# Kernel optimization log

Measured on AMD Instinct MI355X. Metric: run time of the kernel, lower is better.

The kernel has to match this reference:

```python
import jax, jax.numpy as jnp
import numpy as np

N = 50000      # nodes
E = 800000     # edges
IN_DIM = 256
H = 128
OUT_DIM = 64
DEPTH = 3
NEG_SLOPE = 0.2  # DGL GATConv default leaky_relu slope


def setup_inputs() -> dict:
    key = jax.random.key(0)
    ks = jax.random.split(key, 20)
    def nrm(k, shape, fan_in):
        return jax.random.normal(k, shape, jnp.float32) / jnp.sqrt(jnp.float32(fan_in))
    x = jax.random.normal(ks[0], (N, IN_DIM), jnp.float32)
    src = jax.random.randint(ks[1], (E,), 0, N, jnp.int32)
    dst = jax.random.randint(ks[2], (E,), 0, N, jnp.int32)
    # weights stored as [in, out] (y = x @ W + b)
    inp = dict(
        x=x, src=src, dst=dst,
        wx_W=nrm(ks[3], (IN_DIM, H), IN_DIM), wx_b=jnp.zeros((H,), jnp.float32),
        gat_W=nrm(ks[4], (DEPTH, H, H), H), gat_b=jnp.zeros((DEPTH, H), jnp.float32),
        attn_l=nrm(ks[5], (DEPTH, H), H), attn_r=nrm(ks[6], (DEPTH, H), H),
        ig_W=nrm(ks[7], (DEPTH, 2 * H, H), 2 * H), ig_b=jnp.zeros((DEPTH, H), jnp.float32),
        fg_W=nrm(ks[8], (DEPTH, 2 * H, H), 2 * H), fg_b=jnp.zeros((DEPTH, H), jnp.float32),
        og_W=nrm(ks[9], (DEPTH, 2 * H, H), 2 * H), og_b=jnp.zeros((DEPTH, H), jnp.float32),
        st_W=nrm(ks[10], (DEPTH, 2 * H, H), 2 * H), st_b=jnp.zeros((DEPTH, H), jnp.float32),
        out_W=nrm(ks[11], (H, OUT_DIM), H), out_b=jnp.zeros((OUT_DIM,), jnp.float32),
    )
    return inp


def _breadth(h, W, b, a_l, a_r, src, dst):
    """DGL GATConv with 1 head + tanh activation; mean over heads is identity."""
    z = h @ W                                  # [N, H]
    el = z @ a_l                               # [N]
    er = z @ a_r                               # [N]
    e = jax.nn.leaky_relu(el[src] + er[dst], NEG_SLOPE)   # [E]
    # edge softmax over incoming edges of each dst node
    emax = jax.ops.segment_max(e, dst, num_segments=N)    # [N]
    emax = jnp.where(jnp.isfinite(emax), emax, 0.0)       # guard isolated nodes
    ex = jnp.exp(e - emax[dst])                            # [E]
    denom = jax.ops.segment_sum(ex, dst, num_segments=N)   # [N]
    alpha = ex / jnp.maximum(denom, 1e-16)[dst]             # [E]
    agg = jax.ops.segment_sum(alpha[:, None] * z[src], dst, num_segments=N)  # [N, H]
    return jnp.tanh(agg + b)


def reference(x, src, dst, wx_W, wx_b, gat_W, gat_b, attn_l, attn_r,
              ig_W, ig_b, fg_W, fg_b, og_W, og_b, st_W, st_b, out_W, out_b):
    h0 = x @ wx_W + wx_b                       # [N, H]
    h = h0
    collector = []
    for i in range(DEPTH):
        h = _breadth(h, gat_W[i], gat_b[i], attn_l[i], attn_r[i], src, dst)
        collector.append(h)
    mu = h0
    c = jnp.zeros_like(mu)
    for i in range(DEPTH):
        hm = jnp.concatenate([collector[i], mu], axis=1)   # [N, 2H]
        ig = jax.nn.sigmoid(hm @ ig_W[i] + ig_b[i])
        fg = jax.nn.sigmoid(hm @ fg_W[i] + fg_b[i])
        og = jax.nn.sigmoid(hm @ og_W[i] + og_b[i])
        c_tilde = jnp.tanh(hm @ st_W[i] + st_b[i])
        c = fg * c + ig * c_tilde
        mu = og * jnp.tanh(c)
    return jax.nn.relu(mu @ out_W + out_b)     # [N, OUT_DIM]
```

## Files before the change

### kernel.cpp

```cpp
#include <hip/hip_runtime.h>
#include <math.h>
#include <type_traits>

#define NN 50000
#define EE 800000
#define IN_D 256
#define HH 128
#define OUT_D 64
#define DEPTH 3
#define BK 512
#define NBK 98

typedef unsigned short u16;
typedef __bf16  bf16x8 __attribute__((ext_vector_type(8)));
typedef short   short8 __attribute__((ext_vector_type(8)));
typedef float   f32x4  __attribute__((ext_vector_type(4)));

__device__ __forceinline__ u16 f2b(float f){
    unsigned u = __float_as_uint(f);
    u += 0x7fff + ((u>>16)&1);
    return (u16)(u>>16);
}
__device__ __forceinline__ float b2f(u16 h){ return __uint_as_float(((unsigned)h)<<16); }

#define LOG2E 1.4426950408889634f
#if __has_builtin(__builtin_amdgcn_exp2f)
__device__ __forceinline__ float fexp2(float x){ return __builtin_amdgcn_exp2f(x); }
#else
__device__ __forceinline__ float fexp2(float x){ return exp2f(x); }
#endif
#if __has_builtin(__builtin_amdgcn_rcpf)
__device__ __forceinline__ float frcp(float x){ return __builtin_amdgcn_rcpf(x); }
#else
__device__ __forceinline__ float frcp(float x){ return 1.f/x; }
#endif
__device__ __forceinline__ float sigm(float x){ return frcp(1.f + fexp2(-x*LOG2E)); }
__device__ __forceinline__ float ftanh(float x){
    float ax = fabsf(x);
    float u = fexp2(ax * (-2.f*LOG2E));
    float r = (1.f - u) * frcp(1.f + u);
    return copysignf(r, x);
}

enum { EPI_BF=0, EPI_RELU=1, EPI_ZEL=2 };

template<int EPI, int WAVES, int CT, int K, typename TA>
__global__ __launch_bounds__(WAVES*64, 4) void rgemm_k(
    const TA* __restrict__ A1,
    const u16* __restrict__ Bp,
    const float* __restrict__ b1, const float* __restrict__ b2,
    void* __restrict__ Out, float* __restrict__ aux1, float* __restrict__ aux2,
    int Nrows)
{
    constexpr int TH = WAVES*64;
    constexpr int KS = K/32;
    constexpr int M  = WAVES*CT*16;
    __shared__ u16 As[64*K];
    __shared__ float elp[(EPI==EPI_ZEL)?64*WAVES:1];
    __shared__ float erp[(EPI==EPI_ZEL)?64*WAVES:1];

    const int tid = threadIdx.x;
    const int rb  = blockIdx.x*64;

    constexpr int CHUNKS = 64*K/(TH*8);
    #pragma unroll
    for (int c = 0; c < CHUNKS; ++c) {
        int h = (tid + c*TH)*8;
        int row = h / K, kk = h % K;
        int grow = rb + row; if (grow >= Nrows) grow = Nrows-1;
        short8 v;
        if constexpr (std::is_same<TA,float>::value) {
            const float* p = (const float*)A1 + (size_t)grow*K + kk;
            float4 x0 = *(const float4*)p;
            float4 x1 = *(const float4*)(p+4);
            v[0]=(short)f2b(x0.x); v[1]=(short)f2b(x0.y); v[2]=(short)f2b(x0.z); v[3]=(short)f2b(x0.w);
            v[4]=(short)f2b(x1.x); v[5]=(short)f2b(x1.y); v[6]=(short)f2b(x1.z); v[7]=(short)f2b(x1.w);
        } else {
            v = *(const short8*)((const u16*)A1 + (size_t)grow*K + kk);
        }
        int byte = row*(K*2) + ((kk*2) ^ ((row&7)<<4));
        *(short8*)((char*)As + byte) = v;
    }
    __syncthreads();

    const int lane = tid & 63, w = tid >> 6;
    const int ml = lane & 15, ksel = lane >> 4;
    f32x4 acc[4][CT] = {};
    #pragma unroll
    for (int ks = 0; ks < KS; ++ks) {
        bf16x8 a[4];
        #pragma unroll
        for (int rt = 0; rt < 4; ++rt) {
            int row = rt*16 + ml;
            int byte = row*(K*2) + (((ks*32 + ksel*8)*2) ^ ((row&7)<<4));
            a[rt] = *(const bf16x8*)((const char*)As + byte);
        }
        #pragma unroll
        for (int j = 0; j < CT; ++j) {
            int ctg = j*WAVES + w;
            bf16x8 b = *(const bf16x8*)(Bp + (((size_t)(ctg*KS + ks))<<9) + lane*8);
            #pragma unroll
            for (int rt = 0; rt < 4; ++rt)
                acc[rt][j] = __builtin_amdgcn_mfma_f32_16x16x32_bf16(a[rt], b, acc[rt][j], 0,0,0);
        }
    }

    if constexpr (EPI==EPI_BF || EPI==EPI_RELU) {
        #pragma unroll
        for (int rt = 0; rt < 4; ++rt)
        #pragma unroll
        for (int r = 0; r < 4; ++r) {
            int row = rb + rt*16 + ksel*4 + r;
            if (row >= Nrows) continue;
            #pragma unroll
            for (int j = 0; j < CT; ++j) {
                int gc = (j*WAVES + w)*16 + ml;
                float vv = acc[rt][j][r] + b1[gc];
                if (EPI==EPI_BF) ((u16*)Out)[(size_t)row*M + gc]   = f2b(vv);
                else             ((float*)Out)[(size_t)row*M + gc] = fmaxf(vv, 0.f);
            }
        }
    } else {
        float pel[4][4] = {}, per[4][4] = {};
        #pragma unroll
        for (int j = 0; j < CT; ++j) {
            int gc = (j*WAVES + w)*16 + ml;
            float alc = b1[gc], arc = b2[gc];
            #pragma unroll
            for (int rt = 0; rt < 4; ++rt)
            #pragma unroll
            for (int r = 0; r < 4; ++r) {
                int row = rb + rt*16 + ksel*4 + r;
                float vv = acc[rt][j][r];
                if (row < Nrows) ((u16*)Out)[(size_t)row*HH + gc] = f2b(vv);
                pel[rt][r] = fmaf(vv, alc, pel[rt][r]);
                per[rt][r] = fmaf(vv, arc, per[rt][r]);
            }
        }
        #pragma unroll
        for (int msk = 1; msk < 16; msk <<= 1)
            #pragma unroll
            for (int rt = 0; rt < 4; ++rt)
            #pragma unroll
            for (int r = 0; r < 4; ++r) {
                pel[rt][r] += __shfl_xor(pel[rt][r], msk);
                per[rt][r] += __shfl_xor(per[rt][r], msk);
            }
        if (ml == 0) {
            #pragma unroll
            for (int rt = 0; rt < 4; ++rt)
            #pragma unroll
            for (int r = 0; r < 4; ++r) {
                int lr = rt*16 + ksel*4 + r;
                elp[lr*WAVES + w] = pel[rt][r];
                erp[lr*WAVES + w] = per[rt][r];
            }
        }
        __syncthreads();
        if (tid < 64) {
            int row = rb + tid;
            if (row < Nrows) {
                float s1 = 0.f, s2 = 0.f;
                #pragma unroll
                for (int wv = 0; wv < WAVES; ++wv) { s1 += elp[tid*WAVES+wv]; s2 += erp[tid*WAVES+wv]; }
                aux1[row] = s1; aux2[row] = s2;
            }
        }
    }
}

__global__ __launch_bounds__(512, 4) void depth_k(
    const u16* __restrict__ coll0, const u16* __restrict__ coll1, const u16* __restrict__ coll2,
    u16* __restrict__ mu,
    const u16* __restrict__ gateP,
    const float* __restrict__ igb, const float* __restrict__ stb,
    const float* __restrict__ fgb, const float* __restrict__ ogb,
    int Nrows)
{
    __shared__ u16 As[64*HH];
    __shared__ u16 Ms[64*HH];
    const int tid = threadIdx.x;
    const int rb  = blockIdx.x*64;
    const int lane = tid & 63, w = tid >> 6;
    const int ml = lane & 15, ksel = lane >> 4;
    const int gcg = w*16 + ml;

    #pragma unroll
    for (int c = 0; c < 2; ++c) {
        int h = (tid + c*512)*8;
        int row = h >> 7, kk = h & 127;
        int grow = rb + row; if (grow >= Nrows) grow = Nrows-1;
        short8 v = *(const short8*)(mu + (size_t)grow*HH + kk);
        *(short8*)((char*)Ms + row*256 + ((kk*2) ^ ((row&7)<<4))) = v;
    }

    float cc[4][4];
    const u16* colls[3] = {coll0, coll1, coll2};

    for (int i = 0; i < DEPTH; ++i) {
        const u16* coll = colls[i];
        #pragma unroll
        for (int c = 0; c < 2; ++c) {
            int h = (tid + c*512)*8;
            int row = h >> 7, kk = h & 127;
            int grow = rb + row; if (grow >= Nrows) grow = Nrows-1;
            short8 v = *(const short8*)(coll + (size_t)grow*HH + kk);
            *(short8*)((char*)As + row*256 + ((kk*2) ^ ((row&7)<<4))) = v;
        }
        __syncthreads();

        f32x4 acc[4][4] = {};
        #pragma unroll
        for (int ks = 0; ks < 8; ++ks) {
            const char* Sb = (ks < 4) ? (const char*)As : (const char*)Ms;
            int kk2 = ((ks & 3)*32 + ksel*8)*2;
            bf16x8 a[4];
            #pragma unroll
            for (int rt = 0; rt < 4; ++rt) {
                int row = rt*16 + ml;
                a[rt] = *(const bf16x8*)(Sb + row*256 + (kk2 ^ ((row&7)<<4)));
            }
            #pragma unroll
            for (int j = 0; j < 4; ++j) {
                bf16x8 b = *(const bf16x8*)(gateP + (size_t)i*131072 + (j*8 + w)*4096 + ks*512 + lane*8);
                #pragma unroll
                for (int rt = 0; rt < 4; ++rt)
                    acc[rt][j] = __builtin_amdgcn_mfma_f32_16x16x32_bf16(a[rt], b, acc[rt][j], 0,0,0);
            }
        }
        __syncthreads();

        float bi = igb[i*HH + gcg], bs = stb[i*HH + gcg];
        float bf_ = fgb[i*HH + gcg], bo = ogb[i*HH + gcg];
        #pragma unroll
        for (int rt = 0; rt < 4; ++rt)
        #pragma unroll
        for (int r = 0; r < 4; ++r) {
            float ig = sigm (acc[rt][0][r] + bi);
            float st = ftanh(acc[rt][1][r] + bs);
            float fg = sigm (acc[rt][2][r] + bf_);
            float og = sigm (acc[rt][3][r] + bo);
            float P  = ig * st;
            float cn = (i == 0) ? P : fmaf(fg, cc[rt][r], P);
            cc[rt][r] = cn;
            float mun = og * ftanh(cn);
            int lrow = rt*16 + ksel*4 + r;
            *(u16*)((char*)Ms + lrow*256 + ((gcg*2) ^ ((lrow&7)<<4))) = f2b(mun);
        }
        __syncthreads();
    }

    #pragma unroll
    for (int c = 0; c < 2; ++c) {
        int h = (tid + c*512)*8;
        int row = h >> 7, kk = h & 127;
        int grow = rb + row;
        if (grow < Nrows) {
            short8 v = *(const short8*)((const char*)Ms + row*256 + ((kk*2) ^ ((row&7)<<4)));
            *(short8*)(mu + (size_t)grow*HH + kk) = v;
        }
    }
}

struct PK  { const float* s; u16* d; int K; int Mc; };
struct PKs { PK t[17]; };
__global__ __launch_bounds__(256) void pack_k(PKs ps){
    const PK t = ps.t[blockIdx.y];
    int o = blockIdx.x*256 + threadIdx.x;
    if (o >= t.K * t.Mc) return;
    int i = o & 7, lane = (o>>3) & 63, rst = o >> 9;
    int KS = t.K >> 5;
    int ks = rst % KS, ct = rst / KS;
    int col = ct*16 + (lane & 15);
    int k   = ks*32 + (lane>>4)*8 + i;
    t.d[o] = f2b(t.s[(size_t)k*t.Mc + col]);
}

__global__ __launch_bounds__(256) void binh_k(const int* __restrict__ dst, int* __restrict__ bcnt){
    __shared__ int h[NBK];
    int t = threadIdx.x;
    if (t < NBK) h[t] = 0;
    __syncthreads();
    int base = blockIdx.x*4096;
    #pragma unroll
    for (int c = 0; c < 16; ++c){ int e = base + c*256 + t; if (e < EE) atomicAdd(&h[dst[e]>>9], 1); }
    __syncthreads();
    if (t < NBK && h[t]) atomicAdd(&bcnt[t], h[t]);
}
__global__ __launch_bounds__(128) void bscan_k(const int* __restrict__ bcnt,
                                               int* __restrict__ bbase, int* __restrict__ gcur){
    __shared__ int s[128];
    int t = threadIdx.x;
    int v = (t < NBK) ? bcnt[t] : 0;
    s[t] = v; __syncthreads();
    for (int off=1; off<128; off<<=1){ int x = (t>=off)? s[t-off] : 0; __syncthreads(); s[t] += x; __syncthreads(); }
    if (t < NBK){ bbase[t] = s[t]-v; gcur[t] = s[t]-v; }
}
__global__ __launch_bounds__(256) void binsc_k(const int* __restrict__ dst, const int* __restrict__ src,
                                               int* __restrict__ gcur, unsigned* __restrict__ staged){
    __shared__ int h[NBK], bb[NBK], lc[NBK];
    int t = threadIdx.x;
    if (t < NBK){ h[t]=0; lc[t]=0; }
    __syncthreads();
    int base = blockIdx.x*4096;
    int d[16], s[16];
    #pragma unroll
    for (int c = 0; c < 16; ++c){
        int e = base + c*256 + t; d[c] = -1;
        if (e < EE){ d[c] = dst[e]; s[c] = src[e]; atomicAdd(&h[d[c]>>9], 1); }
    }
    __syncthreads();
    if (t < NBK && h[t]) bb[t] = atomicAdd(&gcur[t], h[t]);
    __syncthreads();
    #pragma unroll
    for (int c = 0; c < 16; ++c) if (d[c] >= 0){
        int b = d[c]>>9;
        int r = atomicAdd(&lc[b], 1);
        staged[bb[b] + r] = ((unsigned)(d[c] & 511) << 16) | (unsigned)s[c];
    }
}
__global__ __launch_bounds__(BK) void build_k(const int* __restrict__ bcnt, const int* __restrict__ bbase,
                                              const unsigned* __restrict__ staged,
                                              int* __restrict__ rp, int* __restrict__ deg, u16* __restrict__ srcs){
    __shared__ int soff[BK], cur[BK];
    int t = threadIdx.x, bk = blockIdx.x;
    int n0 = bk*BK;
    soff[t] = 0; cur[t] = 0;
    __syncthreads();
    int cb = bcnt[bk], eb = bbase[bk];
    for (int j = t; j < cb; j += BK) atomicAdd(&soff[staged[eb+j]>>16], 1);
    __syncthreads();
    int d0 = soff[t];
    for (int off=1; off<BK; off<<=1){ int x = (t>=off)? soff[t-off] : 0; __syncthreads(); soff[t] += x; __syncthreads(); }
    int ex = soff[t] - d0;
    __syncthreads();
    soff[t] = ex;
    int n = n0 + t;
    if (n < NN){ deg[n] = d0; rp[n] = eb + ex; }
    __syncthreads();
    for (int j = t; j < cb; j += BK){
        unsigned p = staged[eb+j];
        int l = p >> 16;
        int r = atomicAdd(&cur[l], 1);
        srcs[eb + soff[l] + r] = (u16)(p & 0xffff);
    }
}

__global__ __launch_bounds__(256) void gat_k(
    const u16* __restrict__ z, const float* __restrict__ el, const float* __restrict__ er,
    const u16* __restrict__ srcs, const int* __restrict__ rp, const int* __restrict__ deg,
    const float* __restrict__ bias, u16* __restrict__ hout)
{
    int n = blockIdx.x*4 + (threadIdx.x>>6);
    if (n >= NN) return;
    int lane = threadIdx.x & 63;
    int start = rp[n], cnt = deg[n];
    float ern = er[n];
    const int slot = lane >> 4;
    const int ch   = (lane & 15) * 8;
    float acc[8] = {};

    if (cnt <= 64) {
        float v = -1e30f; int s_reg = 0;
        if (lane < cnt) {
            s_reg = srcs[start + lane];
            float tv = el[s_reg] + ern;
            v = tv >= 0.f ? tv : 0.2f*tv;
        }
        float m = v;
        #pragma unroll
        for (int off=1; off<64; off<<=1) m = fmaxf(m, __shfl_xor(m, off));
        float a = (lane < cnt) ? fexp2((v - m)*LOG2E) : 0.f;
        float ss = a;
        #pragma unroll
        for (int off=1; off<64; off<<=1) ss += __shfl_xor(ss, off);
        float a_reg = a * frcp(fmaxf(ss, 1e-16f));

        const int cntp = (cnt + 7) & ~7;
        for (int i = slot; i < cntp; i += 8) {
            float w0 = __shfl(a_reg, i),   w1 = __shfl(a_reg, i+4);
            int   s0 = __shfl(s_reg, i),   s1 = __shfl(s_reg, i+4);
            short8 v0 = *(const short8*)(z + (size_t)s0*HH + ch);
            short8 v1 = *(const short8*)(z + (size_t)s1*HH + ch);
            #pragma unroll
            for (int j=0;j<8;j++) acc[j] = fmaf(w1, b2f((u16)v1[j]), fmaf(w0, b2f((u16)v0[j]), acc[j]));
        }
    } else {
        float m = -1e30f;
        for (int i=lane; i<cnt; i+=64){ float tv = el[srcs[start+i]] + ern; tv = tv>=0.f?tv:0.2f*tv; m = fmaxf(m, tv); }
        #pragma unroll
        for (int off=1; off<64; off<<=1) m = fmaxf(m, __shfl_xor(m, off));
        float ss = 0.f;
        for (int i=lane; i<cnt; i+=64){ float tv = el[srcs[start+i]] + ern; tv = tv>=0.f?tv:0.2f*tv; ss += fexp2((tv-m)*LOG2E); }
        #pragma unroll
        for (int off=1; off<64; off<<=1) ss += __shfl_xor(ss, off);
        float inv = frcp(fmaxf(ss, 1e-16f));
        for (int i=slot; i<cnt; i+=4) {
            int sn = srcs[start+i];
            float tv = el[sn] + ern; tv = tv>=0.f?tv:0.2f*tv;
            float w0 = fexp2((tv-m)*LOG2E) * inv;
            short8 v0 = *(const short8*)(z + (size_t)sn*HH + ch);
            #pragma unroll
            for (int j=0;j<8;j++) acc[j] = fmaf(w0, b2f((u16)v0[j]), acc[j]);
        }
    }
    #pragma unroll
    for (int j=0;j<8;j++){ acc[j] += __shfl_xor(acc[j],16); acc[j] += __shfl_xor(acc[j],32); }
    if (slot == 0) {
        short8 o8;
        #pragma unroll
        for (int j=0;j<8;j++) o8[j] = (short)f2b(ftanh(acc[j] + bias[ch+j]));
        *(short8*)(hout + (size_t)n*HH + ch) = o8;
    }
}

extern "C" void kernel_launch(void* const* d_in, const int* in_sizes, int n_in,
                              void* d_out, int out_size, void* d_ws, size_t ws_size,
                              hipStream_t stream)
{
    const float* x    = (const float*)d_in[0];
    const int*   src  = (const int*)d_in[1];
    const int*   dst  = (const int*)d_in[2];
    const float* wxW  = (const float*)d_in[3];
    const float* wxb  = (const float*)d_in[4];
    const float* gatW = (const float*)d_in[5];
    const float* gatb = (const float*)d_in[6];
    const float* attl = (const float*)d_in[7];
    const float* attr = (const float*)d_in[8];
    const float* igW  = (const float*)d_in[9];
    const float* igb  = (const float*)d_in[10];
    const float* fgW  = (const float*)d_in[11];
    const float* fgb  = (const float*)d_in[12];
    const float* ogW  = (const float*)d_in[13];
    const float* ogb  = (const float*)d_in[14];
    const float* stW  = (const float*)d_in[15];
    const float* stb  = (const float*)d_in[16];
    const float* outW = (const float*)d_in[17];
    const float* outb = (const float*)d_in[18];

    char* w = (char*)d_ws;
    auto alloc = [&](size_t bytes)->char* { char* p = w; w += (bytes + 255) & ~(size_t)255; return p; };
    const size_t NH = (size_t)NN * HH;
    u16*      muB    = (u16*)alloc(NH*2);
    u16*      zB     = (u16*)alloc(NH*2);
    u16*      coll0  = (u16*)alloc(NH*2);
    u16*      coll1  = (u16*)alloc(NH*2);
    u16*      coll2  = (u16*)alloc(NH*2);
    float*    el     = (float*)alloc((size_t)NN*4);
    float*    er     = (float*)alloc((size_t)NN*4);
    unsigned* staged = (unsigned*)alloc((size_t)EE*4);
    u16*      srcs   = (u16*)alloc((size_t)EE*2);
    int*      deg    = (int*)alloc((size_t)NN*4);
    int*      rp     = (int*)alloc((size_t)NN*4);
    int*      bcnt   = (int*)alloc(128*4);
    int*      bbase  = (int*)alloc(128*4);
    int*      gcur   = (int*)alloc(128*4);
    u16*      bpool  = (u16*)alloc(483328*2);
    u16* wxP   = bpool;
    u16* gatP  = bpool + 32768;
    u16* gateP = bpool + 81920;
    u16* outP  = bpool + 475136;
    u16* coll[3] = {coll0, coll1, coll2};

    PKs ps;
    ps.t[0] = {wxW, wxP, IN_D, HH};
    for (int i=0;i<3;i++) ps.t[1+i]  = {gatW + (size_t)i*HH*HH,   gatP  + i*16384,           HH,   HH};
    for (int i=0;i<3;i++) ps.t[4+i]  = {igW  + (size_t)i*2*HH*HH, gateP + i*131072,          2*HH, HH};
    for (int i=0;i<3;i++) ps.t[7+i]  = {stW  + (size_t)i*2*HH*HH, gateP + i*131072 + 32768,  2*HH, HH};
    for (int i=0;i<3;i++) ps.t[10+i] = {fgW  + (size_t)i*2*HH*HH, gateP + i*131072 + 65536,  2*HH, HH};
    for (int i=0;i<3;i++) ps.t[13+i] = {ogW  + (size_t)i*2*HH*HH, gateP + i*131072 + 98304,  2*HH, HH};
    ps.t[16] = {outW, outP, HH, OUT_D};
    pack_k<<<dim3(128,17), 256, 0, stream>>>(ps);

    hipMemsetAsync(bcnt, 0, 128*4, stream);
    const int gE = (EE + 4095) / 4096;
    binh_k <<<gE, 256, 0, stream>>>(dst, bcnt);
    bscan_k<<<1, 128, 0, stream>>>(bcnt, bbase, gcur);
    binsc_k<<<gE, 256, 0, stream>>>(dst, src, gcur, staged);
    build_k<<<NBK, BK, 0, stream>>>(bcnt, bbase, staged, rp, deg, srcs);

    const int gN = (NN + 63) / 64;
    const int gA = (NN + 3) / 4;

    rgemm_k<EPI_BF,4,2,IN_D,float><<<gN, 256, 0, stream>>>(
        x, wxP, wxb, nullptr, muB, nullptr, nullptr, NN);

    const u16* hin = muB;
    for (int i = 0; i < DEPTH; ++i) {
        rgemm_k<EPI_ZEL,4,2,HH,u16><<<gN, 256, 0, stream>>>(
            hin, gatP + i*16384, attl + i*HH, attr + i*HH, zB, el, er, NN);
        gat_k<<<gA, 256, 0, stream>>>(zB, el, er, srcs, rp, deg, gatb + i*HH, coll[i]);
        hin = coll[i];
    }

    depth_k<<<gN, 512, 0, stream>>>(coll0, coll1, coll2, muB, gateP,
                                    igb, stb, fgb, ogb, NN);

    rgemm_k<EPI_RELU,4,1,HH,u16><<<gN, 256, 0, stream>>>(
        muB, outP, outb, nullptr, (float*)d_out, nullptr, nullptr, NN);
}
```

Before: 321.0 us.

## Fuse output projection into LSTM depth kernel and split gate GEMM into two halves

The final ReLU output GEMM now runs inside depth_k, so the mu tile stays in shared memory and the separate launch plus the global write and re-read of mu go away. The gate GEMM is split into two passes (input/state gates, then forget/output gates), which halves the live accumulators to lower register pressure. Launch bounds drop from 4 to 3 blocks per SM and the barriers move. Only half the waves do the output projection, so that tail is partly idle.

```diff
diff --git a/kernel.cpp b/kernel.cpp
--- a/kernel.cpp
+++ b/kernel.cpp
@@ -169,12 +169,13 @@
     }
 }
 
-__global__ __launch_bounds__(512, 4) void depth_k(
+__global__ __launch_bounds__(512, 3) void depth_k(
     const u16* __restrict__ coll0, const u16* __restrict__ coll1, const u16* __restrict__ coll2,
-    u16* __restrict__ mu,
-    const u16* __restrict__ gateP,
+    const u16* __restrict__ mu0,
+    const u16* __restrict__ gateP, const u16* __restrict__ outP,
     const float* __restrict__ igb, const float* __restrict__ stb,
     const float* __restrict__ fgb, const float* __restrict__ ogb,
+    const float* __restrict__ outb, float* __restrict__ Out,
     int Nrows)
 {
     __shared__ u16 As[64*HH];
@@ -190,15 +191,15 @@
         int h = (tid + c*512)*8;
         int row = h >> 7, kk = h & 127;
         int grow = rb + row; if (grow >= Nrows) grow = Nrows-1;
-        short8 v = *(const short8*)(mu + (size_t)grow*HH + kk);
+        short8 v = *(const short8*)(mu0 + (size_t)grow*HH + kk);
         *(short8*)((char*)Ms + row*256 + ((kk*2) ^ ((row&7)<<4))) = v;
     }
 
     float cc[4][4];
-    const u16* colls[3] = {coll0, coll1, coll2};
-
+    #pragma unroll
     for (int i = 0; i < DEPTH; ++i) {
-        const u16* coll = colls[i];
+        const u16* coll = (i==0) ? coll0 : (i==1) ? coll1 : coll2;
+        __syncthreads();
         #pragma unroll
         for (int c = 0; c < 2; ++c) {
             int h = (tid + c*512)*8;
@@ -209,55 +210,97 @@
         }
         __syncthreads();
 
-        f32x4 acc[4][4] = {};
-        #pragma unroll
-        for (int ks = 0; ks < 8; ++ks) {
-            const char* Sb = (ks < 4) ? (const char*)As : (const char*)Ms;
-            int kk2 = ((ks & 3)*32 + ksel*8)*2;
+        float P_[4][4];
+        {
+            f32x4 acc[4][2] = {};
+            #pragma unroll
+            for (int ks = 0; ks < 8; ++ks) {
+                const char* Sb = (ks < 4) ? (const char*)As : (const char*)Ms;
+                int kk2 = ((ks & 3)*32 + ksel*8)*2;
+                bf16x8 a[4];
+                #pragma unroll
+                for (int rt = 0; rt < 4; ++rt) {
+                    int row = rt*16 + ml;
+                    a[rt] = *(const bf16x8*)(Sb + row*256 + (kk2 ^ ((row&7)<<4)));
+                }
+                #pragma unroll
+                for (int g = 0; g < 2; ++g) {
+                    bf16x8 b = *(const bf16x8*)(gateP + (size_t)i*131072 + (g*8 + w)*4096 + ks*512 + lane*8);
+                    #pragma unroll
+                    for (int rt = 0; rt < 4; ++rt)
+                        acc[rt][g] = __builtin_amdgcn_mfma_f32_16x16x32_bf16(a[rt], b, acc[rt][g], 0,0,0);
+                }
+            }
+            float bi = igb[i*HH + gcg], bs = stb[i*HH + gcg];
+            #pragma unroll
+            for (int rt = 0; rt < 4; ++rt)
+            #pragma unroll
+            for (int r = 0; r < 4; ++r)
+                P_[rt][r] = sigm(acc[rt][0][r] + bi) * ftanh(acc[rt][1][r] + bs);
+        }
+        {
+            f32x4 acc[4][2] = {};
+            #pragma unroll
+            for (int ks = 0; ks < 8; ++ks) {
+                const char* Sb = (ks < 4) ? (const char*)As : (const char*)Ms;
+                int kk2 = ((ks & 3)*32 + ksel*8)*2;
+                bf16x8 a[4];
+                #pragma unroll
+                for (int rt = 0; rt < 4; ++rt) {
+                    int row = rt*16 + ml;
+                    a[rt] = *(const bf16x8*)(Sb + row*256 + (kk2 ^ ((row&7)<<4)));
+                }
+                #pragma unroll
+                for (int g = 0; g < 2; ++g) {
+                    bf16x8 b = *(const bf16x8*)(gateP + (size_t)i*131072 + ((g+2)*8 + w)*4096 + ks*512 + lane*8);
+                    #pragma unroll
+                    for (int rt = 0; rt < 4; ++rt)
+                        acc[rt][g] = __builtin_amdgcn_mfma_f32_16x16x32_bf16(a[rt], b, acc[rt][g], 0,0,0);
+                }
+            }
+            float bf_ = fgb[i*HH + gcg], bo = ogb[i*HH + gcg];
+            __syncthreads();
+            #pragma unroll
+            for (int rt = 0; rt < 4; ++rt)
+            #pragma unroll
+            for (int r = 0; r < 4; ++r) {
+                float fg = sigm(acc[rt][0][r] + bf_);
+                float og = sigm(acc[rt][1][r] + bo);
+                float cn = (i == 0) ? P_[rt][r] : fmaf(fg, cc[rt][r], P_[rt][r]);
+                cc[rt][r] = cn;
+                float mun = og * ftanh(cn);
+                int lrow = rt*16 + ksel*4 + r;
+                *(u16*)((char*)Ms + lrow*256 + ((gcg*2) ^ ((lrow&7)<<4))) = f2b(mun);
+            }
+        }
+    }
+    __syncthreads();
+
+    if (w < 4) {
+        f32x4 acc[4] = {};
+        #pragma unroll
+        for (int ks = 0; ks < 4; ++ks) {
+            int kk2 = (ks*32 + ksel*8)*2;
             bf16x8 a[4];
             #pragma unroll
             for (int rt = 0; rt < 4; ++rt) {
                 int row = rt*16 + ml;
-                a[rt] = *(const bf16x8*)(Sb + row*256 + (kk2 ^ ((row&7)<<4)));
-            }
-            #pragma unroll
-            for (int j = 0; j < 4; ++j) {
-                bf16x8 b = *(const bf16x8*)(gateP + (size_t)i*131072 + (j*8 + w)*4096 + ks*512 + lane*8);
-                #pragma unroll
-                for (int rt = 0; rt < 4; ++rt)
-                    acc[rt][j] = __builtin_amdgcn_mfma_f32_16x16x32_bf16(a[rt], b, acc[rt][j], 0,0,0);
-            }
-        }
-        __syncthreads();
-
-        float bi = igb[i*HH + gcg], bs = stb[i*HH + gcg];
-        float bf_ = fgb[i*HH + gcg], bo = ogb[i*HH + gcg];
+                a[rt] = *(const bf16x8*)((const char*)Ms + row*256 + (kk2 ^ ((row&7)<<4)));
+            }
+            bf16x8 b = *(const bf16x8*)(outP + (size_t)((w*4 + ks)<<9) + lane*8);
+            #pragma unroll
+            for (int rt = 0; rt < 4; ++rt)
+                acc[rt] = __builtin_amdgcn_mfma_f32_16x16x32_bf16(a[rt], b, acc[rt], 0,0,0);
+        }
+        int gc = w*16 + ml;
+        float bb = outb[gc];
         #pragma unroll
         for (int rt = 0; rt < 4; ++rt)
         #pragma unroll
         for (int r = 0; r < 4; ++r) {
-            float ig = sigm (acc[rt][0][r] + bi);
-            float st = ftanh(acc[rt][1][r] + bs);
-            float fg = sigm (acc[rt][2][r] + bf_);
-            float og = sigm (acc[rt][3][r] + bo);
-            float P  = ig * st;
-            float cn = (i == 0) ? P : fmaf(fg, cc[rt][r], P);
-            cc[rt][r] = cn;
-            float mun = og * ftanh(cn);
-            int lrow = rt*16 + ksel*4 + r;
-            *(u16*)((char*)Ms + lrow*256 + ((gcg*2) ^ ((lrow&7)<<4))) = f2b(mun);
-        }
-        __syncthreads();
-    }
-
-    #pragma unroll
-    for (int c = 0; c < 2; ++c) {
-        int h = (tid + c*512)*8;
-        int row = h >> 7, kk = h & 127;
-        int grow = rb + row;
-        if (grow < Nrows) {
-            short8 v = *(const short8*)((const char*)Ms + row*256 + ((kk*2) ^ ((row&7)<<4)));
-            *(short8*)(mu + (size_t)grow*HH + kk) = v;
+            int row = rb + rt*16 + ksel*4 + r;
+            if (row < Nrows)
+                Out[(size_t)row*OUT_D + gc] = fmaxf(acc[rt][r] + bb, 0.f);
         }
     }
 }
@@ -493,9 +536,6 @@
         hin = coll[i];
     }
 
-    depth_k<<<gN, 512, 0, stream>>>(coll0, coll1, coll2, muB, gateP,
-                                    igb, stb, fgb, ogb, NN);
-
-    rgemm_k<EPI_RELU,4,1,HH,u16><<<gN, 256, 0, stream>>>(
-        muB, outP, outb, nullptr, (float*)d_out, nullptr, nullptr, NN);
-}
+    depth_k<<<gN, 512, 0, stream>>>(coll0, coll1, coll2, muB, gateP, outP,
+                                    igb, stb, fgb, ogb, outb, (float*)d_out, NN);
+}
```

Result: faster. 309.7 us (-3.5%).

## Fuse output projection into depth kernel and prefetch next collector tile

Applied to the files above, without the earlier changes.

Fuses the final ReLU output GEMM into the LSTM-style depth kernel, so mu stays in shared memory and is neither written back to global nor re-read by a separate launch. It also register-prefetches the next depth's collector rows while the current depth computes, and unrolls the depth loop. Occupancy hint drops from 4 to 3 blocks per CU to make room for the extra registers, which may reduce latency hiding.

```diff
diff --git a/kernel.cpp b/kernel.cpp
--- a/kernel.cpp
+++ b/kernel.cpp
@@ -169,12 +169,13 @@
     }
 }
 
-__global__ __launch_bounds__(512, 4) void depth_k(
+__global__ __launch_bounds__(512, 3) void depth_k(
     const u16* __restrict__ coll0, const u16* __restrict__ coll1, const u16* __restrict__ coll2,
-    u16* __restrict__ mu,
-    const u16* __restrict__ gateP,
+    const u16* __restrict__ mu0,
+    const u16* __restrict__ gateP, const u16* __restrict__ outP,
     const float* __restrict__ igb, const float* __restrict__ stb,
     const float* __restrict__ fgb, const float* __restrict__ ogb,
+    const float* __restrict__ outb, float* __restrict__ Out,
     int Nrows)
 {
     __shared__ u16 As[64*HH];
@@ -185,28 +186,28 @@
     const int ml = lane & 15, ksel = lane >> 4;
     const int gcg = w*16 + ml;
 
-    #pragma unroll
-    for (int c = 0; c < 2; ++c) {
-        int h = (tid + c*512)*8;
-        int row = h >> 7, kk = h & 127;
-        int grow = rb + row; if (grow >= Nrows) grow = Nrows-1;
-        short8 v = *(const short8*)(mu + (size_t)grow*HH + kk);
-        *(short8*)((char*)Ms + row*256 + ((kk*2) ^ ((row&7)<<4))) = v;
-    }
+    const int h0_ = tid*8,        h1_ = (tid+512)*8;
+    const int row0 = h0_ >> 7,    kk0 = h0_ & 127;
+    const int row1 = h1_ >> 7,    kk1 = h1_ & 127;
+    int gr0 = rb + row0; if (gr0 >= Nrows) gr0 = Nrows-1;
+    int gr1 = rb + row1; if (gr1 >= Nrows) gr1 = Nrows-1;
+    const size_t off0 = (size_t)gr0*HH + kk0, off1 = (size_t)gr1*HH + kk1;
+    const int dst0 = row0*256 + ((kk0*2) ^ ((row0&7)<<4));
+    const int dst1 = row1*256 + ((kk1*2) ^ ((row1&7)<<4));
+
+    *(short8*)((char*)Ms + dst0) = *(const short8*)(mu0 + off0);
+    *(short8*)((char*)Ms + dst1) = *(const short8*)(mu0 + off1);
+    short8 pf0 = *(const short8*)(coll0 + off0);
+    short8 pf1 = *(const short8*)(coll0 + off1);
 
     float cc[4][4];
-    const u16* colls[3] = {coll0, coll1, coll2};
-
+    #pragma unroll
     for (int i = 0; i < DEPTH; ++i) {
-        const u16* coll = colls[i];
-        #pragma unroll
-        for (int c = 0; c < 2; ++c) {
-            int h = (tid + c*512)*8;
-            int row = h >> 7, kk = h & 127;
-            int grow = rb + row; if (grow >= Nrows) grow = Nrows-1;
-            short8 v = *(const short8*)(coll + (size_t)grow*HH + kk);
-            *(short8*)((char*)As + row*256 + ((kk*2) ^ ((row&7)<<4))) = v;
-        }
+        __syncthreads();
+        *(short8*)((char*)As + dst0) = pf0;
+        *(short8*)((char*)As + dst1) = pf1;
+        if (i == 0) { pf0 = *(const short8*)(coll1 + off0); pf1 = *(const short8*)(coll1 + off1); }
+        if (i == 1) { pf0 = *(const short8*)(coll2 + off0); pf1 = *(const short8*)(coll2 + off1); }
         __syncthreads();
 
         f32x4 acc[4][4] = {};
@@ -221,11 +222,11 @@
                 a[rt] = *(const bf16x8*)(Sb + row*256 + (kk2 ^ ((row&7)<<4)));
             }
             #pragma unroll
-            for (int j = 0; j < 4; ++j) {
-                bf16x8 b = *(const bf16x8*)(gateP + (size_t)i*131072 + (j*8 + w)*4096 + ks*512 + lane*8);
+            for (int g = 0; g < 4; ++g) {
+                bf16x8 b = *(const bf16x8*)(gateP + (size_t)i*131072 + (g*8 + w)*4096 + ks*512 + lane*8);
                 #pragma unroll
                 for (int rt = 0; rt < 4; ++rt)
-                    acc[rt][j] = __builtin_amdgcn_mfma_f32_16x16x32_bf16(a[rt], b, acc[rt][j], 0,0,0);
+                    acc[rt][g] = __builtin_amdgcn_mfma_f32_16x16x32_bf16(a[rt], b, acc[rt][g], 0,0,0);
             }
         }
         __syncthreads();
@@ -247,17 +248,36 @@
             int lrow = rt*16 + ksel*4 + r;
             *(u16*)((char*)Ms + lrow*256 + ((gcg*2) ^ ((lrow&7)<<4))) = f2b(mun);
         }
-        __syncthreads();
-    }
-
-    #pragma unroll
-    for (int c = 0; c < 2; ++c) {
-        int h = (tid + c*512)*8;
-        int row = h >> 7, kk = h & 127;
-        int grow = rb + row;
-        if (grow < Nrows) {
-            short8 v = *(const short8*)((const char*)Ms + row*256 + ((kk*2) ^ ((row&7)<<4)));
-            *(short8*)(mu + (size_t)grow*HH + kk) = v;
+    }
+    __syncthreads();
+
+    {
+        const int ct = w & 3;
+        const int rh = (w >> 2) * 2;
+        f32x4 acc[2] = {};
+        #pragma unroll
+        for (int ks = 0; ks < 4; ++ks) {
+            int kk2 = (ks*32 + ksel*8)*2;
+            bf16x8 a[2];
+            #pragma unroll
+            for (int q = 0; q < 2; ++q) {
+                int row = (rh + q)*16 + ml;
+                a[q] = *(const bf16x8*)((const char*)Ms + row*256 + (kk2 ^ ((row&7)<<4)));
+            }
+            bf16x8 b = *(const bf16x8*)(outP + (size_t)((ct*4 + ks)<<9) + lane*8);
+            #pragma unroll
+            for (int q = 0; q < 2; ++q)
+                acc[q] = __builtin_amdgcn_mfma_f32_16x16x32_bf16(a[q], b, acc[q], 0,0,0);
+        }
+        int gc = ct*16 + ml;
+        float bb = outb[gc];
+        #pragma unroll
+        for (int q = 0; q < 2; ++q)
+        #pragma unroll
+        for (int r = 0; r < 4; ++r) {
+            int row = rb + (rh + q)*16 + ksel*4 + r;
+            if (row < Nrows)
+                Out[(size_t)row*OUT_D + gc] = fmaxf(acc[q][r] + bb, 0.f);
         }
     }
 }
@@ -493,9 +513,6 @@
         hin = coll[i];
     }
 
-    depth_k<<<gN, 512, 0, stream>>>(coll0, coll1, coll2, muB, gateP,
-                                    igb, stb, fgb, ogb, NN);
-
-    rgemm_k<EPI_RELU,4,1,HH,u16><<<gN, 256, 0, stream>>>(
-        muB, outP, outb, nullptr, (float*)d_out, nullptr, nullptr, NN);
-}
+    depth_k<<<gN, 512, 0, stream>>>(coll0, coll1, coll2, muB, gateP, outP,
+                                    igb, stb, fgb, ogb, outb, (float*)d_out, NN);
+}
```

New measurement: 305.2 us. 4.9% less time.
